# Kernel optimization log

Hardware: AMD Instinct MI355X
Metric: run time of the kernel (lower is better)

## Reference

```python
import jax, jax.numpy as jnp
import numpy as np

B, T, C, H = 4, 4096, 1024, 64

def setup_inputs() -> dict:
    key = jax.random.key(0)
    k1, k2, k3, k4, k5 = jax.random.split(key, 5)
    scale = 0.02
    return {
        "x": jax.random.normal(k1, (B, T, C), dtype=jnp.float32),
        "head_bias": jax.random.normal(k2, (T, T), dtype=jnp.float32) * 0.1,
        "w_k": jax.random.normal(k3, (C, H), dtype=jnp.float32) * scale,
        "w_q": jax.random.normal(k4, (C, H), dtype=jnp.float32) * scale,
        "w_v": jax.random.normal(k5, (C, H), dtype=jnp.float32) * scale,
    }

def reference(x, head_bias, w_k, w_q, w_v):
    # x: (B,T,C) ; projections: (B,T,H)
    k = jnp.einsum('btc,ch->bth', x, w_k)
    q = jnp.einsum('btc,ch->bth', x, w_q)
    v = jnp.einsum('btc,ch->bth', x, w_v)
    Tq = x.shape[1]
    # scores: (B,T,T) with RPE bias and causal mask
    scores = jnp.einsum('bqh,bkh->bqk', q, k) * (k.shape[-1] ** -0.5)
    scores = scores + head_bias[None, :, :]
    causal = jnp.tril(jnp.ones((Tq, Tq), dtype=bool))
    scores = jnp.where(causal[None, :, :], scores, -jnp.inf)
    weights = jax.nn.softmax(scores, axis=-1)
    out = jnp.einsum('bqk,bkh->bqh', weights, v)
    return out
```

## Files before the change

kernel.cpp:

```cpp
#include <hip/hip_runtime.h>
#include <hip/hip_bf16.h>


#define T_DIM 4096
#define C_DIM 1024
#define CK    256

typedef __attribute__((ext_vector_type(8))) short s16x8;
typedef __attribute__((ext_vector_type(4))) float f32x4;
typedef __attribute__((ext_vector_type(2))) unsigned int u32x2;
typedef __attribute__((ext_vector_type(4))) unsigned int u32x4;

__device__ __forceinline__ short f2bf(float f) {
    unsigned u = __builtin_bit_cast(unsigned, f);
    u += 0x7FFFu + ((u >> 16) & 1u);
    return (short)(u >> 16);
}
__device__ __forceinline__ unsigned pack2(float a, float b) {
    unsigned ua = __builtin_bit_cast(unsigned, a);
    unsigned ub = __builtin_bit_cast(unsigned, b);
    ua += 0x7FFFu + ((ua >> 16) & 1u);
    ub += 0x7FFFu + ((ub >> 16) & 1u);
    return __builtin_amdgcn_perm(ub, ua, 0x07060302u);
}
__device__ __forceinline__ float bf2f(short s) {
    unsigned u = ((unsigned)(unsigned short)s) << 16;
    return __builtin_bit_cast(float, u);
}
__device__ __forceinline__ int chunk_off(int qt) {
    int g = qt >> 4, r = qt & 15;
    return qt + 8 * g * (g - 1) + r * g;
}

__global__ __launch_bounds__(256) void prep_frag(
    const float* __restrict__ wk, const float* __restrict__ wq,
    const float* __restrict__ wv, short* __restrict__ wfrag)
{
    int ksAll = blockIdx.x, mat = blockIdx.y;
    const float* w = (mat == 0) ? wk : ((mat == 1) ? wq : wv);
    float sc = (mat == 1) ? 0.125f : 1.0f;
    int nt = threadIdx.x >> 6, lane = threadIdx.x & 63;
    int quad = lane >> 4, l15 = lane & 15;
    int h = nt * 16 + l15;
    int cb = ksAll * 32 + quad * 8;
    s16x8 v;
    #pragma unroll
    for (int j = 0; j < 8; ++j) v[j] = f2bf(w[(cb + j) * 64 + h] * sc);
    *(s16x8*)&wfrag[((ksAll * 12 + mat * 4 + nt) * 64 + lane) * 8] = v;
}

union ProjSmem {
    short xs[32][1032];
    struct {
        short comb[2][16][136];
        short vsep[64][40];
    } c;
};

__global__ __launch_bounds__(256, 2) void proj_fused(
    const float* __restrict__ x, const short* __restrict__ wfrag,
    short* __restrict__ qb, short* __restrict__ kfrag, short* __restrict__ vfrag)
{
    __shared__ __align__(16) ProjSmem sm;

    int tid = threadIdx.x;
    int w = tid >> 6, lane = tid & 63;
    int rt = w >> 1, h = w & 1;
    int l15 = lane & 15, quad = lane >> 4;
    int m0 = blockIdx.x * 32;

    s16x8 fA[12], fB[12];
    {
        const s16x8* fb = (const s16x8*)&wfrag[((size_t)(h * 16) * 12 * 64 + lane) * 8];
        #pragma unroll
        for (int f = 0; f < 12; ++f) fA[f] = fb[f * 64];
    }

    #pragma unroll 8
    for (int p = 0; p < 32; ++p) {
        f32x4 v = *(const f32x4*)&x[(size_t)(m0 + p) * C_DIM + tid * 4];
        u32x2 d;
        d[0] = pack2(v[0], v[1]);
        d[1] = pack2(v[2], v[3]);
        *(u32x2*)&sm.xs[p][tid * 4] = d;
    }
    __syncthreads();

    f32x4 acc[12];
    #pragma unroll
    for (int i = 0; i < 12; ++i) acc[i] = (f32x4){0.f, 0.f, 0.f, 0.f};

    #pragma unroll 1
    for (int ks = 0; ks < 16; ks += 2) {
        {
            const s16x8* fb = (const s16x8*)&wfrag[((size_t)(h * 16 + ks + 1) * 12 * 64 + lane) * 8];
            #pragma unroll
            for (int f = 0; f < 12; ++f) fB[f] = fb[f * 64];
        }
        s16x8 af = *(const s16x8*)&sm.xs[rt * 16 + l15][(h * 16 + ks) * 32 + quad * 8];
        #pragma unroll
        for (int f = 0; f < 12; ++f)
            acc[f] = __builtin_amdgcn_mfma_f32_16x16x32_bf16(af, fA[f], acc[f], 0, 0, 0);
        if (ks + 2 < 16) {
            const s16x8* fb = (const s16x8*)&wfrag[((size_t)(h * 16 + ks + 2) * 12 * 64 + lane) * 8];
            #pragma unroll
            for (int f = 0; f < 12; ++f) fA[f] = fb[f * 64];
        }
        s16x8 af2 = *(const s16x8*)&sm.xs[rt * 16 + l15][(h * 16 + ks + 1) * 32 + quad * 8];
        #pragma unroll
        for (int f = 0; f < 12; ++f)
            acc[f] = __builtin_amdgcn_mfma_f32_16x16x32_bf16(af2, fB[f], acc[f], 0, 0, 0);
    }
    __syncthreads();

    if (h == 1) {
        #pragma unroll
        for (int f = 0; f < 8; ++f)
            #pragma unroll
            for (int r = 0; r < 4; ++r)
                sm.c.comb[rt][quad * 4 + r][(f >> 2) * 64 + (f & 3) * 16 + l15] = f2bf(acc[f][r]);
        #pragma unroll
        for (int f = 8; f < 12; ++f)
            #pragma unroll
            for (int r = 0; r < 4; ++r)
                sm.c.vsep[(f & 3) * 16 + l15][rt * 16 + quad * 4 + r] = f2bf(acc[f][r]);
    }
    __syncthreads();
    if (h == 0) {
        #pragma unroll
        for (int f = 0; f < 8; ++f)
            #pragma unroll
            for (int r = 0; r < 4; ++r) {
                int col = (f >> 2) * 64 + (f & 3) * 16 + l15, rr = quad * 4 + r;
                sm.c.comb[rt][rr][col] = f2bf(acc[f][r] + bf2f(sm.c.comb[rt][rr][col]));
            }
        #pragma unroll
        for (int f = 8; f < 12; ++f)
            #pragma unroll
            for (int r = 0; r < 4; ++r) {
                int hh = (f & 3) * 16 + l15, kk = rt * 16 + quad * 4 + r;
                sm.c.vsep[hh][kk] = f2bf(acc[f][r] + bf2f(sm.c.vsep[hh][kk]));
            }
    }
    __syncthreads();

    int b = m0 >> 12, t0 = m0 & 4095;
    int t016 = t0 >> 4, kt32 = t0 >> 5;
    {
        int row = tid >> 3, ch = tid & 7;
        s16x8 v = *(const s16x8*)&sm.c.comb[row >> 4][row & 15][64 + ch * 8];
        *(s16x8*)&qb[(size_t)(m0 + row) * 64 + ch * 8] = v;
    }
    {
        int kt = w & 1, ks = w >> 1;
        s16x8 v = *(const s16x8*)&sm.c.comb[kt][l15][ks * 32 + quad * 8];
        *(s16x8*)&kfrag[(size_t)(((b * 256 + t016 + kt) * 2 + ks) * 64 + lane) * 8] = v;
    }
    {
        int nt = w;
        s16x8 v = *(const s16x8*)&sm.c.vsep[nt * 16 + l15][quad * 8];
        *(s16x8*)&vfrag[(size_t)(((b * 128 + kt32) * 4 + nt) * 64 + lane) * 8] = v;
    }
}

#define LOADK(AK, k0) do {                                                    \
    int _kt16 = (k0) >> 4;                                                    \
    _Pragma("unroll")                                                         \
    for (int _n = 0; _n < 2; ++_n) {                                          \
        const short* _kp = kfb + (size_t)((_kt16 + _n) * 2) * 512 + lane * 8; \
        AK[_n * 2]     = *(const s16x8*)_kp;                                  \
        AK[_n * 2 + 1] = *(const s16x8*)(_kp + 512);                          \
    }                                                                         \
} while (0)

#define LOADV(BV, k0) do {                                                    \
    int _kt32 = (k0) >> 5;                                                    \
    _Pragma("unroll")                                                         \
    for (int _n = 0; _n < 4; ++_n)                                            \
        BV[_n] = *(const s16x8*)(vfb + (size_t)(_kt32 * 4 + _n) * 512 + lane * 8); \
} while (0)

#define SOFT(N, AS, KL, PLO, PHI) do {                                        \
    f32x4 _vb = *(const f32x4*)&blds[l15][(KL) + (N) * 16 + quad * 4];        \
    float _sv[4];                                                             \
    _Pragma("unroll")                                                         \
    for (int _r = 0; _r < 4; ++_r) {                                          \
        _sv[_r] = (AS)[_r] + _vb[_r];                                         \
        if (mask_on && (kabs + (N) * 16 + quad * 4 + _r > strip0 + l15))      \
            _sv[_r] = -__builtin_inff();                                      \
        float _p = __expf(_sv[_r]);                                           \
        _sv[_r] = _p;                                                         \
        l_sum += _p;                                                          \
    }                                                                         \
    PLO = pack2(_sv[0], _sv[1]);                                              \
    PHI = pack2(_sv[2], _sv[3]);                                              \
} while (0)

#define COMPUTEK(AK, BV, k0) do {                                             \
    int _kl = (k0) - kstart;                                                  \
    int kabs = (k0);                                                          \
    f32x4 _aS0 = (f32x4){0.f, 0.f, 0.f, 0.f};                                 \
    f32x4 _aS1 = (f32x4){0.f, 0.f, 0.f, 0.f};                                 \
    _aS0 = __builtin_amdgcn_mfma_f32_16x16x32_bf16(AK[0], aq0, _aS0, 0, 0, 0); \
    _aS0 = __builtin_amdgcn_mfma_f32_16x16x32_bf16(AK[1], aq1, _aS0, 0, 0, 0); \
    _aS1 = __builtin_amdgcn_mfma_f32_16x16x32_bf16(AK[2], aq0, _aS1, 0, 0, 0); \
    _aS1 = __builtin_amdgcn_mfma_f32_16x16x32_bf16(AK[3], aq1, _aS1, 0, 0, 0); \
    unsigned _p0, _p1, _p2, _p3;                                              \
    SOFT(0, _aS0, _kl, _p0, _p1);                                             \
    SOFT(1, _aS1, _kl, _p2, _p3);                                             \
    asm("v_permlane32_swap_b32 %0, %1" : "+v"(_p0), "+v"(_p2));               \
    asm("v_permlane16_swap_b32 %0, %1" : "+v"(_p0), "+v"(_p2));               \
    asm("v_permlane32_swap_b32 %0, %1" : "+v"(_p1), "+v"(_p3));               \
    asm("v_permlane16_swap_b32 %0, %1" : "+v"(_p1), "+v"(_p3));               \
    u32x4 _apu = (u32x4){_p0, _p1, _p2, _p3};                                 \
    s16x8 _ap = __builtin_bit_cast(s16x8, _apu);                              \
    accO[0] = __builtin_amdgcn_mfma_f32_16x16x32_bf16(_ap, BV[0], accO[0], 0, 0, 0); \
    accO[1] = __builtin_amdgcn_mfma_f32_16x16x32_bf16(_ap, BV[1], accO[1], 0, 0, 0); \
    accO[2] = __builtin_amdgcn_mfma_f32_16x16x32_bf16(_ap, BV[2], accO[2], 0, 0, 0); \
    accO[3] = __builtin_amdgcn_mfma_f32_16x16x32_bf16(_ap, BV[3], accO[3], 0, 0, 0); \
} while (0)

__global__ __launch_bounds__(256, 4) void flash_part(
    const short* __restrict__ qb, const short* __restrict__ kfrag,
    const short* __restrict__ vfrag, const float* __restrict__ bias,
    short* __restrict__ po)
{
    int qt = blockIdx.x, c = blockIdx.y;
    if (c > (qt >> 4)) return;
    int q0 = qt * 16;
    int kstart = c * CK;
    int kend = min(kstart + CK, q0 + 16);

    __shared__ __align__(16) float blds[16][260];

    int w = threadIdx.x >> 6, lane = threadIdx.x & 63;
    int b = w;
    int l15 = lane & 15, quad = lane >> 4;
    int strip0 = q0;

    #pragma unroll
    for (int p = 0; p < 4; ++p)
        *(f32x4*)&blds[p * 4 + w][lane * 4] =
            *(const f32x4*)&bias[(size_t)(q0 + p * 4 + w) * T_DIM + kstart + lane * 4];

    const short* qrow = qb + (size_t)(b * T_DIM + strip0 + l15) * 64;
    s16x8 aq0 = *(const s16x8*)(qrow + quad * 8);
    s16x8 aq1 = *(const s16x8*)(qrow + 32 + quad * 8);

    float l_sum = 0.f;
    f32x4 accO[4];
    #pragma unroll
    for (int nt = 0; nt < 4; ++nt) accO[nt] = (f32x4){0.f, 0.f, 0.f, 0.f};

    const short* kfb = kfrag + (size_t)b * 256 * 2 * 512;
    const short* vfb = vfrag + (size_t)b * 128 * 4 * 512;
    bool mask_on = (kend > strip0);

    __syncthreads();

    s16x8 akA[4], akB[4], bvA[4], bvB[4];
    int k0 = kstart;
    LOADK(akA, k0);
    LOADV(bvA, k0);
    while (true) {
        int k1 = k0 + 32;
        bool more = (k1 < kend);
        if (more) { LOADK(akB, k1); LOADV(bvB, k1); }
        COMPUTEK(akA, bvA, k0);
        if (!more) break;
        k0 = k1; k1 = k0 + 32;
        bool more2 = (k1 < kend);
        if (more2) { LOADK(akA, k1); LOADV(bvA, k1); }
        COMPUTEK(akB, bvB, k0);
        if (!more2) break;
        k0 = k1;
    }

    l_sum += __shfl_xor(l_sum, 16, 64);
    l_sum += __shfl_xor(l_sum, 32, 64);

    short* base = po + (size_t)((chunk_off(qt) + c) * 4 + b) * 1040;
    #pragma unroll
    for (int nt = 0; nt < 4; ++nt)
        #pragma unroll
        for (int r = 0; r < 4; ++r)
            base[(quad * 4 + r) * 64 + nt * 16 + l15] = f2bf(accO[nt][r]);
    if (quad == 0) base[1024 + l15] = f2bf(l_sum);
}

__global__ __launch_bounds__(256) void flash_reduce(
    const short* __restrict__ po, float* __restrict__ out)
{
    int idx = blockIdx.x * 256 + threadIdx.x;
    int row = idx >> 3, c8 = idx & 7;
    int b = row >> 12, t = row & 4095;
    int qt = t >> 4, rloc = t & 15;
    int nc = (t >> 8) + 1;
    int off = chunk_off(qt);
    float o[8];
    #pragma unroll
    for (int j = 0; j < 8; ++j) o[j] = 0.f;
    float l = 0.f;
    #pragma unroll 1
    for (int cc = 0; cc < nc; ++cc) {
        const short* base = po + (size_t)((off + cc) * 4 + b) * 1040;
        s16x8 v = *(const s16x8*)&base[rloc * 64 + c8 * 8];
        #pragma unroll
        for (int j = 0; j < 8; ++j) o[j] += bf2f(v[j]);
        l += bf2f(base[1024 + rloc]);
    }
    float inv = 1.0f / l;
    f32x4 r0 = (f32x4){o[0] * inv, o[1] * inv, o[2] * inv, o[3] * inv};
    f32x4 r1 = (f32x4){o[4] * inv, o[5] * inv, o[6] * inv, o[7] * inv};
    float* op = &out[(size_t)row * 64 + c8 * 8];
    *(f32x4*)op = r0;
    *(f32x4*)(op + 4) = r1;
}

extern "C" void kernel_launch(void* const* d_in, const int* in_sizes, int n_in,
                              void* d_out, int out_size, void* d_ws, size_t ws_size,
                              hipStream_t stream) {
    (void)in_sizes; (void)n_in; (void)out_size; (void)ws_size;
    const float* x    = (const float*)d_in[0];
    const float* bias = (const float*)d_in[1];
    const float* wk   = (const float*)d_in[2];
    const float* wq   = (const float*)d_in[3];
    const float* wv   = (const float*)d_in[4];
    float* out = (float*)d_out;

    short* wfrag = (short*)d_ws;
    short* qb    = wfrag + 196608;
    short* kfrag = qb + 1048576;
    short* vfrag = kfrag + 1048576;
    short* po    = vfrag + 1048576;

    prep_frag<<<dim3(32, 3), dim3(256), 0, stream>>>(wk, wq, wv, wfrag);
    proj_fused<<<dim3(512), dim3(256), 0, stream>>>(x, wfrag, qb, kfrag, vfrag);
    flash_part<<<dim3(256, 16), dim3(256), 0, stream>>>(qb, kfrag, vfrag, bias, po);
    flash_reduce<<<dim3(512), dim3(256), 0, stream>>>(po, out);
}
```

Measured before the change: 195.6 us.

## Process two 16-row query tiles per block to reuse K/V fragments

```diff
diff --git a/kernel.cpp b/kernel.cpp
--- a/kernel.cpp
+++ b/kernel.cpp
@@ -180,81 +180,98 @@
         BV[_n] = *(const s16x8*)(vfb + (size_t)(_kt32 * 4 + _n) * 512 + lane * 8); \
 } while (0)
 
-#define SOFT(N, AS, KL, PLO, PHI) do {                                        \
-    f32x4 _vb = *(const f32x4*)&blds[l15][(KL) + (N) * 16 + quad * 4];        \
+#define SOFT(N, AS, KL, RO, Q0S, LS, PLO, PHI) do {                           \
+    f32x4 _vb = *(const f32x4*)&blds[(RO) + l15][(KL) + (N) * 16 + quad * 4]; \
     float _sv[4];                                                             \
     _Pragma("unroll")                                                         \
     for (int _r = 0; _r < 4; ++_r) {                                          \
         _sv[_r] = (AS)[_r] + _vb[_r];                                         \
-        if (mask_on && (kabs + (N) * 16 + quad * 4 + _r > strip0 + l15))      \
+        if (mask_on && (kabs + (N) * 16 + quad * 4 + _r > (Q0S) + l15))       \
             _sv[_r] = -__builtin_inff();                                      \
         float _p = __expf(_sv[_r]);                                           \
         _sv[_r] = _p;                                                         \
-        l_sum += _p;                                                          \
+        LS += _p;                                                             \
     }                                                                         \
     PLO = pack2(_sv[0], _sv[1]);                                              \
     PHI = pack2(_sv[2], _sv[3]);                                              \
 } while (0)
+
+#define PERM4(P0, P1, P2, P3)                                                 \
+    asm("v_permlane32_swap_b32 %0, %1" : "+v"(P0), "+v"(P2));                 \
+    asm("v_permlane16_swap_b32 %0, %1" : "+v"(P0), "+v"(P2));                 \
+    asm("v_permlane32_swap_b32 %0, %1" : "+v"(P1), "+v"(P3));                 \
+    asm("v_permlane16_swap_b32 %0, %1" : "+v"(P1), "+v"(P3));
 
 #define COMPUTEK(AK, BV, k0) do {                                             \
     int _kl = (k0) - kstart;                                                  \
     int kabs = (k0);                                                          \
     f32x4 _aS0 = (f32x4){0.f, 0.f, 0.f, 0.f};                                 \
     f32x4 _aS1 = (f32x4){0.f, 0.f, 0.f, 0.f};                                 \
+    f32x4 _aS2 = (f32x4){0.f, 0.f, 0.f, 0.f};                                 \
+    f32x4 _aS3 = (f32x4){0.f, 0.f, 0.f, 0.f};                                 \
     _aS0 = __builtin_amdgcn_mfma_f32_16x16x32_bf16(AK[0], aq0, _aS0, 0, 0, 0); \
     _aS0 = __builtin_amdgcn_mfma_f32_16x16x32_bf16(AK[1], aq1, _aS0, 0, 0, 0); \
     _aS1 = __builtin_amdgcn_mfma_f32_16x16x32_bf16(AK[2], aq0, _aS1, 0, 0, 0); \
     _aS1 = __builtin_amdgcn_mfma_f32_16x16x32_bf16(AK[3], aq1, _aS1, 0, 0, 0); \
-    unsigned _p0, _p1, _p2, _p3;                                              \
-    SOFT(0, _aS0, _kl, _p0, _p1);                                             \
-    SOFT(1, _aS1, _kl, _p2, _p3);                                             \
-    asm("v_permlane32_swap_b32 %0, %1" : "+v"(_p0), "+v"(_p2));               \
-    asm("v_permlane16_swap_b32 %0, %1" : "+v"(_p0), "+v"(_p2));               \
-    asm("v_permlane32_swap_b32 %0, %1" : "+v"(_p1), "+v"(_p3));               \
-    asm("v_permlane16_swap_b32 %0, %1" : "+v"(_p1), "+v"(_p3));               \
-    u32x4 _apu = (u32x4){_p0, _p1, _p2, _p3};                                 \
-    s16x8 _ap = __builtin_bit_cast(s16x8, _apu);                              \
-    accO[0] = __builtin_amdgcn_mfma_f32_16x16x32_bf16(_ap, BV[0], accO[0], 0, 0, 0); \
-    accO[1] = __builtin_amdgcn_mfma_f32_16x16x32_bf16(_ap, BV[1], accO[1], 0, 0, 0); \
-    accO[2] = __builtin_amdgcn_mfma_f32_16x16x32_bf16(_ap, BV[2], accO[2], 0, 0, 0); \
-    accO[3] = __builtin_amdgcn_mfma_f32_16x16x32_bf16(_ap, BV[3], accO[3], 0, 0, 0); \
+    _aS2 = __builtin_amdgcn_mfma_f32_16x16x32_bf16(AK[0], aq2, _aS2, 0, 0, 0); \
+    _aS2 = __builtin_amdgcn_mfma_f32_16x16x32_bf16(AK[1], aq3, _aS2, 0, 0, 0); \
+    _aS3 = __builtin_amdgcn_mfma_f32_16x16x32_bf16(AK[2], aq2, _aS3, 0, 0, 0); \
+    _aS3 = __builtin_amdgcn_mfma_f32_16x16x32_bf16(AK[3], aq3, _aS3, 0, 0, 0); \
+    unsigned _p0, _p1, _p2, _p3, _p4, _p5, _p6, _p7;                          \
+    SOFT(0, _aS0, _kl, 0, q0, l_sum0, _p0, _p1);                              \
+    SOFT(1, _aS1, _kl, 0, q0, l_sum0, _p2, _p3);                              \
+    SOFT(0, _aS2, _kl, 16, q0 + 16, l_sum1, _p4, _p5);                        \
+    SOFT(1, _aS3, _kl, 16, q0 + 16, l_sum1, _p6, _p7);                        \
+    PERM4(_p0, _p1, _p2, _p3);                                                \
+    PERM4(_p4, _p5, _p6, _p7);                                                \
+    u32x4 _apuA = (u32x4){_p0, _p1, _p2, _p3};                                \
+    u32x4 _apuB = (u32x4){_p4, _p5, _p6, _p7};                                \
+    s16x8 _apA = __builtin_bit_cast(s16x8, _apuA);                            \
+    s16x8 _apB = __builtin_bit_cast(s16x8, _apuB);                            \
+    _Pragma("unroll")                                                         \
+    for (int _n = 0; _n < 4; ++_n) {                                          \
+        accO[_n]     = __builtin_amdgcn_mfma_f32_16x16x32_bf16(_apA, BV[_n], accO[_n],     0, 0, 0); \
+        accO[_n + 4] = __builtin_amdgcn_mfma_f32_16x16x32_bf16(_apB, BV[_n], accO[_n + 4], 0, 0, 0); \
+    }                                                                         \
 } while (0)
 
-__global__ __launch_bounds__(256, 4) void flash_part(
+__global__ __launch_bounds__(256, 3) void flash_part(
     const short* __restrict__ qb, const short* __restrict__ kfrag,
     const short* __restrict__ vfrag, const float* __restrict__ bias,
     short* __restrict__ po)
 {
-    int qt = blockIdx.x, c = blockIdx.y;
-    if (c > (qt >> 4)) return;
-    int q0 = qt * 16;
+    int g = blockIdx.x, c = blockIdx.y;
+    if (c > (g >> 3)) return;
+    int q0 = g * 32;
     int kstart = c * CK;
-    int kend = min(kstart + CK, q0 + 16);
-
-    __shared__ __align__(16) float blds[16][260];
+    int kend = min(kstart + CK, q0 + 32);
+
+    __shared__ __align__(16) float blds[32][269];
 
     int w = threadIdx.x >> 6, lane = threadIdx.x & 63;
     int b = w;
     int l15 = lane & 15, quad = lane >> 4;
-    int strip0 = q0;
-
-    #pragma unroll
-    for (int p = 0; p < 4; ++p)
+
+    #pragma unroll
+    for (int p = 0; p < 8; ++p)
         *(f32x4*)&blds[p * 4 + w][lane * 4] =
             *(const f32x4*)&bias[(size_t)(q0 + p * 4 + w) * T_DIM + kstart + lane * 4];
 
-    const short* qrow = qb + (size_t)(b * T_DIM + strip0 + l15) * 64;
+    const short* qrow = qb + (size_t)(b * T_DIM + q0 + l15) * 64;
     s16x8 aq0 = *(const s16x8*)(qrow + quad * 8);
     s16x8 aq1 = *(const s16x8*)(qrow + 32 + quad * 8);
-
-    float l_sum = 0.f;
-    f32x4 accO[4];
-    #pragma unroll
-    for (int nt = 0; nt < 4; ++nt) accO[nt] = (f32x4){0.f, 0.f, 0.f, 0.f};
+    const short* qrow2 = qrow + 16 * 64;
+    s16x8 aq2 = *(const s16x8*)(qrow2 + quad * 8);
+    s16x8 aq3 = *(const s16x8*)(qrow2 + 32 + quad * 8);
+
+    float l_sum0 = 0.f, l_sum1 = 0.f;
+    f32x4 accO[8];
+    #pragma unroll
+    for (int nt = 0; nt < 8; ++nt) accO[nt] = (f32x4){0.f, 0.f, 0.f, 0.f};
 
     const short* kfb = kfrag + (size_t)b * 256 * 2 * 512;
     const short* vfb = vfrag + (size_t)b * 128 * 4 * 512;
-    bool mask_on = (kend > strip0);
+    bool mask_on = (kend > q0);
 
     __syncthreads();
 
@@ -276,16 +293,26 @@
         k0 = k1;
     }
 
-    l_sum += __shfl_xor(l_sum, 16, 64);
-    l_sum += __shfl_xor(l_sum, 32, 64);
-
-    short* base = po + (size_t)((chunk_off(qt) + c) * 4 + b) * 1040;
+    l_sum0 += __shfl_xor(l_sum0, 16, 64);
+    l_sum0 += __shfl_xor(l_sum0, 32, 64);
+    l_sum1 += __shfl_xor(l_sum1, 16, 64);
+    l_sum1 += __shfl_xor(l_sum1, 32, 64);
+
+    short* baseA = po + (size_t)((chunk_off(g * 2) + c) * 4 + b) * 1040;
     #pragma unroll
     for (int nt = 0; nt < 4; ++nt)
         #pragma unroll
         for (int r = 0; r < 4; ++r)
-            base[(quad * 4 + r) * 64 + nt * 16 + l15] = f2bf(accO[nt][r]);
-    if (quad == 0) base[1024 + l15] = f2bf(l_sum);
+            baseA[(quad * 4 + r) * 64 + nt * 16 + l15] = f2bf(accO[nt][r]);
+    if (quad == 0) baseA[1024 + l15] = f2bf(l_sum0);
+
+    short* baseB = po + (size_t)((chunk_off(g * 2 + 1) + c) * 4 + b) * 1040;
+    #pragma unroll
+    for (int nt = 0; nt < 4; ++nt)
+        #pragma unroll
+        for (int r = 0; r < 4; ++r)
+            baseB[(quad * 4 + r) * 64 + nt * 16 + l15] = f2bf(accO[nt + 4][r]);
+    if (quad == 0) baseB[1024 + l15] = f2bf(l_sum1);
 }
 
 __global__ __launch_bounds__(256) void flash_reduce(
@@ -336,6 +363,6 @@
 
     prep_frag<<<dim3(32, 3), dim3(256), 0, stream>>>(wk, wq, wv, wfrag);
     proj_fused<<<dim3(512), dim3(256), 0, stream>>>(x, wfrag, qb, kfrag, vfrag);
-    flash_part<<<dim3(256, 16), dim3(256), 0, stream>>>(qb, kfrag, vfrag, bias, po);
+    flash_part<<<dim3(128, 16), dim3(256), 0, stream>>>(qb, kfrag, vfrag, bias, po);
     flash_reduce<<<dim3(512), dim3(256), 0, stream>>>(po, out);
 }
```

Result: no change. 193.1 us (-1.3%).
